# Optimization experiments

Measured on AMD Instinct MI355X. Metric: run time of the kernel, lower is better.

Reference implementation:

```python
import jax, jax.numpy as jnp
import numpy as np

B, S, HID = 2, 2048, 2048
H, HKV, DH = 32, 8, 64
GROUPS = H // HKV
SCALE = DH ** -0.5
ROPE_THETA = 10000.0
NEG_INF = jnp.finfo(jnp.float32).min


def setup_inputs() -> dict:
    key = jax.random.key(0)
    ks = jax.random.split(key, 6)
    hidden_states = jax.random.normal(ks[0], (B, S, HID), dtype=jnp.float32)
    # true rotary embeddings (HF Llama style): inv_freq over half dim, duplicated
    inv_freq = 1.0 / (ROPE_THETA ** (np.arange(0, DH, 2, dtype=np.float32) / DH))
    freqs = np.arange(S, dtype=np.float32)[:, None] * inv_freq[None, :]  # [S, DH/2]
    emb = np.concatenate([freqs, freqs], axis=-1)                        # [S, DH]
    cos = jnp.broadcast_to(jnp.asarray(np.cos(emb), jnp.float32), (B, S, DH))
    sin = jnp.broadcast_to(jnp.asarray(np.sin(emb), jnp.float32), (B, S, DH))
    # additive causal mask [1,1,S,S]
    causal = jnp.tril(jnp.ones((S, S), dtype=bool))
    attention_mask = jnp.where(causal, 0.0, NEG_INF)[None, None].astype(jnp.float32)
    std = 0.02
    Wq = jax.random.normal(ks[1], (H * DH, HID), dtype=jnp.float32) * std
    Wk = jax.random.normal(ks[2], (HKV * DH, HID), dtype=jnp.float32) * std
    Wv = jax.random.normal(ks[3], (HKV * DH, HID), dtype=jnp.float32) * std
    Wo = jax.random.normal(ks[4], (HID, H * DH), dtype=jnp.float32) * std
    return {"hidden_states": hidden_states, "cos": cos, "sin": sin,
            "attention_mask": attention_mask, "Wq": Wq, "Wk": Wk, "Wv": Wv, "Wo": Wo}


def _rotate_half(x):
    x1, x2 = jnp.split(x, 2, axis=-1)
    return jnp.concatenate([-x2, x1], axis=-1)


def reference(hidden_states, cos, sin, attention_mask, Wq, Wk, Wv, Wo):
    b, s, _ = hidden_states.shape
    # projections -> [B, H(kv), S, DH]
    q = (hidden_states @ Wq.T).reshape(b, s, H, DH).transpose(0, 2, 1, 3)
    k = (hidden_states @ Wk.T).reshape(b, s, HKV, DH).transpose(0, 2, 1, 3)
    v = (hidden_states @ Wv.T).reshape(b, s, HKV, DH).transpose(0, 2, 1, 3)
    # RoPE (cos/sin: [B,S,DH] -> broadcast over head axis)
    c = cos[:, None, :, :]
    sn = sin[:, None, :, :]
    q = q * c + _rotate_half(q) * sn
    k = k * c + _rotate_half(k) * sn
    # GQA: repeat kv heads
    k = jnp.repeat(k, GROUPS, axis=1)  # [B,H,S,DH]
    v = jnp.repeat(v, GROUPS, axis=1)
    # eager attention: full [B,H,S,S] scores in memory
    scores = jnp.einsum('bhqd,bhkd->bhqk', q, k) * SCALE + attention_mask[:, :, :, :s]
    attn = jax.nn.softmax(scores, axis=-1)
    out = jnp.einsum('bhqk,bhkd->bhqd', attn, v)
    out = out.transpose(0, 2, 1, 3).reshape(b, s, H * DH)
    return out @ Wo.T
```

## Files before the change

### kernel.cpp

```cpp
#include <hip/hip_runtime.h>
#include <hip/hip_bf16.h>
#include <cstdint>
#include <cstddef>

#define B_    2
#define S_    2048
#define HID_  2048
#define H_    32
#define HKV_  8
#define DH_   64
#define SC2_  0.1803368801111244f

typedef __bf16 bf16;
typedef bf16  bf16x2 __attribute__((ext_vector_type(2)));
typedef bf16  bf16x4 __attribute__((ext_vector_type(4)));
typedef bf16  bf16x8 __attribute__((ext_vector_type(8)));
typedef float f32x4  __attribute__((ext_vector_type(4)));
typedef float f32x16 __attribute__((ext_vector_type(16)));

typedef __attribute__((address_space(3))) uint32_t  lds_u32_t;
typedef __attribute__((address_space(1))) const uint32_t glob_u32_t;

__device__ __forceinline__ void async16(const void* g, void* l) {
    __builtin_amdgcn_global_load_lds((glob_u32_t*)g, (lds_u32_t*)l, 16, 0, 0);
}

__device__ __forceinline__ bf16x8 cvt8(float4 a, float4 b) {
    bf16x8 r;
    r[0] = (bf16)a.x; r[1] = (bf16)a.y; r[2] = (bf16)a.z; r[3] = (bf16)a.w;
    r[4] = (bf16)b.x; r[5] = (bf16)b.y; r[6] = (bf16)b.z; r[7] = (bf16)b.w;
    return r;
}

__device__ __forceinline__ uint32_t pkbf(float a, float b) {
    bf16x2 t; t[0] = (bf16)a; t[1] = (bf16)b;
    return __builtin_bit_cast(uint32_t, t);
}
__device__ __forceinline__ bf16x8 mk8(uint32_t a, uint32_t b, uint32_t c, uint32_t d) {
    union { uint32_t u[4]; bf16x8 v; } t;
    t.u[0] = a; t.u[1] = b; t.u[2] = c; t.u[3] = d;
    return t.v;
}

__global__ __launch_bounds__(256) void cvt_all_kernel(
    const float* __restrict__ X,  const float* __restrict__ Wq,
    const float* __restrict__ Wk, const float* __restrict__ Wv,
    const float* __restrict__ Wo,
    bf16* __restrict__ Xb,  bf16* __restrict__ Wqb, bf16* __restrict__ Wkb,
    bf16* __restrict__ Wvb, bf16* __restrict__ Wob)
{
    const int i = blockIdx.x * 256 + threadIdx.x;
    const float* src; bf16* dst; int off;
    if (i < 1048576)      { src = X;  dst = Xb;  off = i; }
    else if (i < 1572864) { src = Wq; dst = Wqb; off = i - 1048576; }
    else if (i < 1703936) { src = Wk; dst = Wkb; off = i - 1572864; }
    else if (i < 1835008) { src = Wv; dst = Wvb; off = i - 1703936; }
    else                  { src = Wo; dst = Wob; off = i - 1835008; }
    float4 a = ((const float4*)src)[2 * off];
    float4 b = ((const float4*)src)[2 * off + 1];
    ((bf16x8*)dst)[off] = cvt8(a, b);
}

__global__ __launch_bounds__(256) void gemm_qkv_kernel(
    const bf16* __restrict__ A,
    const bf16* __restrict__ Wqb, const bf16* __restrict__ Wkb,
    const bf16* __restrict__ Wvb,
    const float* __restrict__ cs, const float* __restrict__ sn,
    bf16* __restrict__ Qo, bf16* __restrict__ Ko, bf16* __restrict__ Vt)
{
    __shared__ bf16 a_lds[128 * 64];
    __shared__ bf16 b_lds[128 * 64];

    const int tid  = threadIdx.x;
    const int wave = tid >> 6;
    const int lane = tid & 63;
    const int quad = lane >> 4;
    const int l16  = lane & 15;
    const int wm   = wave >> 1;
    const int wn   = wave & 1;
    const int m0   = blockIdx.x * 128;
    const int n0   = blockIdx.y * 128;

    f32x4 acc[4][4];
    #pragma unroll
    for (int mt = 0; mt < 4; ++mt)
        #pragma unroll
        for (int nt = 0; nt < 4; ++nt)
            acc[mt][nt] = (f32x4){0.f, 0.f, 0.f, 0.f};

    int srow[4], sgcol[4];
    const bf16* browp[4];
    #pragma unroll
    for (int i = 0; i < 4; ++i) {
        const int e = tid * 8 + i * 2048;
        srow[i] = e >> 6;
        const int chunk = (e >> 3) & 7;
        sgcol[i] = (chunk ^ (srow[i] & 7)) << 3;
        const int n = n0 + srow[i];
        browp[i] = (n < 2048) ? (Wqb + (size_t)n * HID_)
                 : (n < 2560) ? (Wkb + (size_t)(n - 2048) * HID_)
                              : (Wvb + (size_t)(n - 2560) * HID_);
    }

    for (int k0 = 0; k0 < HID_; k0 += 64) {
        #pragma unroll
        for (int i = 0; i < 4; ++i) {
            async16(A + (size_t)(m0 + srow[i]) * HID_ + k0 + sgcol[i],
                    &a_lds[tid * 8 + i * 2048]);
            async16(browp[i] + k0 + sgcol[i],
                    &b_lds[tid * 8 + i * 2048]);
        }
        __syncthreads();
        #pragma unroll
        for (int ks = 0; ks < 2; ++ks) {
            bf16x8 af[4], bfr[4];
            #pragma unroll
            for (int mt = 0; mt < 4; ++mt) {
                const int row = wm * 64 + mt * 16 + l16;
                const int c = (ks * 4 + quad) ^ (row & 7);
                af[mt] = *(const bf16x8*)(&a_lds[row * 64 + c * 8]);
            }
            #pragma unroll
            for (int nt = 0; nt < 4; ++nt) {
                const int row = wn * 64 + nt * 16 + l16;
                const int c = (ks * 4 + quad) ^ (row & 7);
                bfr[nt] = *(const bf16x8*)(&b_lds[row * 64 + c * 8]);
            }
            #pragma unroll
            for (int mt = 0; mt < 4; ++mt)
                #pragma unroll
                for (int nt = 0; nt < 4; ++nt)
                    acc[mt][nt] = __builtin_amdgcn_mfma_f32_16x16x32_bf16(
                        af[mt], bfr[nt], acc[mt][nt], 0, 0, 0);
        }
        __syncthreads();
    }

    const int nw = n0 + wn * 64;
    const int d  = l16;
    #pragma unroll
    for (int mt = 0; mt < 4; ++mt) {
        #pragma unroll
        for (int r = 0; r < 4; ++r) {
            const int m  = m0 + wm * 64 + mt * 16 + quad * 4 + r;
            const int bb = m >> 11;
            const int ss = m & (S_ - 1);
            const float v0 = acc[mt][0][r], v1 = acc[mt][1][r];
            const float v2 = acc[mt][2][r], v3 = acc[mt][3][r];
            if (nw < 2048) {
                const int h = nw >> 6;
                bf16* dp = Qo + ((size_t)(bb * H_ + h) * S_ + ss) * DH_;
                const float* cp = cs + ((size_t)bb * S_ + ss) * DH_;
                const float* sp = sn + ((size_t)bb * S_ + ss) * DH_;
                dp[ 0 + d] = (bf16)(v0 * cp[ 0 + d] - v2 * sp[ 0 + d]);
                dp[16 + d] = (bf16)(v1 * cp[16 + d] - v3 * sp[16 + d]);
                dp[32 + d] = (bf16)(v2 * cp[32 + d] + v0 * sp[32 + d]);
                dp[48 + d] = (bf16)(v3 * cp[48 + d] + v1 * sp[48 + d]);
            } else if (nw < 2560) {
                const int h = (nw - 2048) >> 6;
                bf16* dp = Ko + ((size_t)(bb * HKV_ + h) * S_ + ss) * DH_;
                const float* cp = cs + ((size_t)bb * S_ + ss) * DH_;
                const float* sp = sn + ((size_t)bb * S_ + ss) * DH_;
                dp[ 0 + d] = (bf16)(v0 * cp[ 0 + d] - v2 * sp[ 0 + d]);
                dp[16 + d] = (bf16)(v1 * cp[16 + d] - v3 * sp[16 + d]);
                dp[32 + d] = (bf16)(v2 * cp[32 + d] + v0 * sp[32 + d]);
                dp[48 + d] = (bf16)(v3 * cp[48 + d] + v1 * sp[48 + d]);
            } else {
                const int h = (nw - 2560) >> 6;
                bf16* dp = Vt + ((size_t)(bb * HKV_ + h) * DH_) * S_ + ss;
                dp[(size_t)( 0 + d) * S_] = (bf16)v0;
                dp[(size_t)(16 + d) * S_] = (bf16)v1;
                dp[(size_t)(32 + d) * S_] = (bf16)v2;
                dp[(size_t)(48 + d) * S_] = (bf16)v3;
            }
        }
    }
}

__global__ __launch_bounds__(256) void gemm_out_kernel(
    const bf16* __restrict__ A, const bf16* __restrict__ Wb,
    float* __restrict__ Y)
{
    __shared__ bf16 a_lds[128 * 64];
    __shared__ bf16 b_lds[128 * 64];

    const int tid  = threadIdx.x;
    const int wave = tid >> 6;
    const int lane = tid & 63;
    const int quad = lane >> 4;
    const int l16  = lane & 15;
    const int wm   = wave >> 1;
    const int wn   = wave & 1;
    const int m0   = blockIdx.x * 128;
    const int n0   = blockIdx.y * 128;

    f32x4 acc[4][4];
    #pragma unroll
    for (int mt = 0; mt < 4; ++mt)
        #pragma unroll
        for (int nt = 0; nt < 4; ++nt)
            acc[mt][nt] = (f32x4){0.f, 0.f, 0.f, 0.f};

    int srow[4], sgcol[4];
    #pragma unroll
    for (int i = 0; i < 4; ++i) {
        const int e = tid * 8 + i * 2048;
        srow[i] = e >> 6;
        const int chunk = (e >> 3) & 7;
        sgcol[i] = (chunk ^ (srow[i] & 7)) << 3;
    }

    for (int k0 = 0; k0 < HID_; k0 += 64) {
        #pragma unroll
        for (int i = 0; i < 4; ++i) {
            async16(A + (size_t)(m0 + srow[i]) * HID_ + k0 + sgcol[i],
                    &a_lds[tid * 8 + i * 2048]);
            async16(Wb + (size_t)(n0 + srow[i]) * HID_ + k0 + sgcol[i],
                    &b_lds[tid * 8 + i * 2048]);
        }
        __syncthreads();
        #pragma unroll
        for (int ks = 0; ks < 2; ++ks) {
            bf16x8 af[4], bfr[4];
            #pragma unroll
            for (int mt = 0; mt < 4; ++mt) {
                const int row = wm * 64 + mt * 16 + l16;
                const int c = (ks * 4 + quad) ^ (row & 7);
                af[mt] = *(const bf16x8*)(&a_lds[row * 64 + c * 8]);
            }
            #pragma unroll
            for (int nt = 0; nt < 4; ++nt) {
                const int row = wn * 64 + nt * 16 + l16;
                const int c = (ks * 4 + quad) ^ (row & 7);
                bfr[nt] = *(const bf16x8*)(&b_lds[row * 64 + c * 8]);
            }
            #pragma unroll
            for (int mt = 0; mt < 4; ++mt)
                #pragma unroll
                for (int nt = 0; nt < 4; ++nt)
                    acc[mt][nt] = __builtin_amdgcn_mfma_f32_16x16x32_bf16(
                        af[mt], bfr[nt], acc[mt][nt], 0, 0, 0);
        }
        __syncthreads();
    }

    #pragma unroll
    for (int mt = 0; mt < 4; ++mt)
        #pragma unroll
        for (int nt = 0; nt < 4; ++nt)
            #pragma unroll
            for (int r = 0; r < 4; ++r) {
                const int m = m0 + wm * 64 + mt * 16 + quad * 4 + r;
                const int n = n0 + wn * 64 + nt * 16 + l16;
                Y[(size_t)m * HID_ + n] = acc[mt][nt][r];
            }
}

__global__ __launch_bounds__(256) void attn_kernel(
    const bf16* __restrict__ Q, const bf16* __restrict__ K,
    const bf16* __restrict__ Vt, bf16* __restrict__ O)
{
    __shared__ bf16 k_lds[2][64 * 64];
    __shared__ bf16 v_lds[2][64 * 64];

    const int tid  = threadIdx.x;
    const int wave = tid >> 6;
    const int lane = tid & 63;
    const int l32  = lane & 31;
    const int half = lane >> 5;
    const int h  = blockIdx.y;
    const int b  = blockIdx.z;
    const int hkv = h >> 2;

    const bf16* Qg = Q  + (size_t)(b * H_ + h) * S_ * DH_;
    const bf16* Kg = K  + (size_t)(b * HKV_ + hkv) * S_ * DH_;
    const bf16* Vg = Vt + ((size_t)(b * HKV_ + hkv) * DH_) * S_;

    const int srow0  = tid >> 3;
    const int scolsw = ((tid & 7) ^ ((tid >> 3) & 7)) << 3;

    #pragma unroll 1
    for (int ph = 0; ph < 2; ++ph) {
        const int qt  = ph == 0 ? (int)blockIdx.x : (15 - (int)blockIdx.x);
        const int q0  = qt * 128;
        const int qb0 = q0 + wave * 32;
        const int qa  = qb0 + l32;

        bf16x8 qf[4];
        #pragma unroll
        for (int c = 0; c < 4; ++c)
            qf[c] = *(const bf16x8*)(Qg + (size_t)(qb0 + l32) * DH_ + c * 16 + half * 8);

        f32x16 o_acc[2];
        #pragma unroll
        for (int dt = 0; dt < 2; ++dt)
            #pragma unroll
            for (int e = 0; e < 16; ++e) o_acc[dt][e] = 0.f;
        float m_i = -1e30f, l_i = 0.f;

        const int nkt = 2 * qt + 2;

        #pragma unroll
        for (int i = 0; i < 2; ++i) {
            const int row = srow0 + i * 32;
            async16(Kg + (size_t)row * DH_ + scolsw, &k_lds[0][tid * 8 + i * 2048]);
            async16(Vg + (size_t)row * S_  + scolsw, &v_lds[0][tid * 8 + i * 2048]);
        }
        __syncthreads();

        for (int kt = 0; kt < nkt; ++kt) {
            if (kt + 1 < nkt) {
                bf16* kb = k_lds[(kt + 1) & 1];
                bf16* vb = v_lds[(kt + 1) & 1];
                #pragma unroll
                for (int i = 0; i < 2; ++i) {
                    const int row = srow0 + i * 32;
                    async16(Kg + (size_t)((kt + 1) * 64 + row) * DH_ + scolsw,
                            kb + tid * 8 + i * 2048);
                    async16(Vg + (size_t)row * S_ + (kt + 1) * 64 + scolsw,
                            vb + tid * 8 + i * 2048);
                }
            }

            if (kt * 64 <= qb0 + 31) {
                const bf16* kb = k_lds[kt & 1];
                const bf16* vb = v_lds[kt & 1];
                const bool act1 = (kt * 64 + 32) <= (qb0 + 31);

                bf16x8 vf[2][4];
                #pragma unroll
                for (int dt = 0; dt < 2; ++dt)
                    #pragma unroll
                    for (int c = 0; c < 4; ++c) {
                        const int row = dt * 32 + l32;
                        const int col = ((2 * c + half) ^ (row & 7)) << 3;
                        vf[dt][c] = *(const bf16x8*)(vb + row * 64 + col);
                    }

                f32x16 s0, s1;
                {
                    bf16x8 kf[4];
                    #pragma unroll
                    for (int c = 0; c < 4; ++c) {
                        const int row = l32;
                        const int col = ((2 * c + half) ^ (row & 7)) << 3;
                        kf[c] = *(const bf16x8*)(kb + row * 64 + col);
                    }
                    f32x16 a;
                    #pragma unroll
                    for (int e = 0; e < 16; ++e) a[e] = 0.f;
                    #pragma unroll
                    for (int c = 0; c < 4; ++c)
                        a = __builtin_amdgcn_mfma_f32_32x32x16_bf16(kf[c], qf[c], a, 0, 0, 0);
                    s0 = a;
                }
                if (act1) {
                    bf16x8 kf[4];
                    #pragma unroll
                    for (int c = 0; c < 4; ++c) {
                        const int row = 32 + l32;
                        const int col = ((2 * c + half) ^ (row & 7)) << 3;
                        kf[c] = *(const bf16x8*)(kb + row * 64 + col);
                    }
                    f32x16 a;
                    #pragma unroll
                    for (int e = 0; e < 16; ++e) a[e] = 0.f;
                    #pragma unroll
                    for (int c = 0; c < 4; ++c)
                        a = __builtin_amdgcn_mfma_f32_32x32x16_bf16(kf[c], qf[c], a, 0, 0, 0);
                    s1 = a;
                }

                {
                    const bool full0 = (kt * 64 + 31) <= qb0;
                    #pragma unroll
                    for (int e = 0; e < 16; ++e) {
                        float v = s0[e] * SC2_;
                        if (!full0) {
                            const int kp = kt * 64 + (e & 3) + 8 * (e >> 2) + 4 * half;
                            v = (kp <= qa) ? v : -1e30f;
                        }
                        s0[e] = v;
                    }
                }
                if (act1) {
                    const bool full1 = (kt * 64 + 63) <= qb0;
                    #pragma unroll
                    for (int e = 0; e < 16; ++e) {
                        float v = s1[e] * SC2_;
                        if (!full1) {
                            const int kp = kt * 64 + 32 + (e & 3) + 8 * (e >> 2) + 4 * half;
                            v = (kp <= qa) ? v : -1e30f;
                        }
                        s1[e] = v;
                    }
                }

                float mx = -1e30f;
                #pragma unroll
                for (int e = 0; e < 16; ++e) mx = fmaxf(mx, s0[e]);
                if (act1)
                    #pragma unroll
                    for (int e = 0; e < 16; ++e) mx = fmaxf(mx, s1[e]);
                mx = fmaxf(mx, __shfl_xor(mx, 32));
                const float mn = fmaxf(m_i, mx);
                const float al = exp2f(m_i - mn);
                m_i = mn;
                float sm = 0.f;
                #pragma unroll
                for (int e = 0; e < 16; ++e) {
                    const float p = exp2f(s0[e] - mn);
                    s0[e] = p; sm += p;
                }
                if (act1)
                    #pragma unroll
                    for (int e = 0; e < 16; ++e) {
                        const float p = exp2f(s1[e] - mn);
                        s1[e] = p; sm += p;
                    }
                sm += __shfl_xor(sm, 32);
                l_i = l_i * al + sm;
                #pragma unroll
                for (int dt = 0; dt < 2; ++dt)
                    #pragma unroll
                    for (int e = 0; e < 16; ++e) o_acc[dt][e] *= al;

                bf16x8 pf[4];
                {
                    uint32_t d0 = pkbf(s0[0],  s0[1]),  d1 = pkbf(s0[2],  s0[3]);
                    uint32_t d2 = pkbf(s0[4],  s0[5]),  d3 = pkbf(s0[6],  s0[7]);
                    uint32_t d4 = pkbf(s0[8],  s0[9]),  d5 = pkbf(s0[10], s0[11]);
                    uint32_t d6 = pkbf(s0[12], s0[13]), d7 = pkbf(s0[14], s0[15]);
                    uint32_t x0 = __shfl_xor((int)d0, 32), x1 = __shfl_xor((int)d1, 32);
                    uint32_t x2 = __shfl_xor((int)d2, 32), x3 = __shfl_xor((int)d3, 32);
                    uint32_t x4 = __shfl_xor((int)d4, 32), x5 = __shfl_xor((int)d5, 32);
                    uint32_t x6 = __shfl_xor((int)d6, 32), x7 = __shfl_xor((int)d7, 32);
                    pf[0] = half ? mk8(x2, x3, d2, d3) : mk8(d0, d1, x0, x1);
                    pf[1] = half ? mk8(x6, x7, d6, d7) : mk8(d4, d5, x4, x5);
                }
                if (act1) {
                    uint32_t d0 = pkbf(s1[0],  s1[1]),  d1 = pkbf(s1[2],  s1[3]);
                    uint32_t d2 = pkbf(s1[4],  s1[5]),  d3 = pkbf(s1[6],  s1[7]);
                    uint32_t d4 = pkbf(s1[8],  s1[9]),  d5 = pkbf(s1[10], s1[11]);
                    uint32_t d6 = pkbf(s1[12], s1[13]), d7 = pkbf(s1[14], s1[15]);
                    uint32_t x0 = __shfl_xor((int)d0, 32), x1 = __shfl_xor((int)d1, 32);
                    uint32_t x2 = __shfl_xor((int)d2, 32), x3 = __shfl_xor((int)d3, 32);
                    uint32_t x4 = __shfl_xor((int)d4, 32), x5 = __shfl_xor((int)d5, 32);
                    uint32_t x6 = __shfl_xor((int)d6, 32), x7 = __shfl_xor((int)d7, 32);
                    pf[2] = half ? mk8(x2, x3, d2, d3) : mk8(d0, d1, x0, x1);
                    pf[3] = half ? mk8(x6, x7, d6, d7) : mk8(d4, d5, x4, x5);
                }

                const int nc = act1 ? 4 : 2;
                #pragma unroll
                for (int c = 0; c < 4; ++c) {
                    if (c >= nc) break;
                    #pragma unroll
                    for (int dt = 0; dt < 2; ++dt)
                        o_acc[dt] = __builtin_amdgcn_mfma_f32_32x32x16_bf16(
                            vf[dt][c], pf[c], o_acc[dt], 0, 0, 0);
                }
            }
            __syncthreads();
        }

        const float inv = 1.f / l_i;
        bf16* op = O + ((size_t)(b * S_ + qa) * H_ + h) * DH_;
        #pragma unroll
        for (int dt = 0; dt < 2; ++dt)
            #pragma unroll
            for (int g = 0; g < 4; ++g) {
                bf16x4 ov;
                #pragma unroll
                for (int r = 0; r < 4; ++r) ov[r] = (bf16)(o_acc[dt][g * 4 + r] * inv);
                *(bf16x4*)(op + dt * 32 + g * 8 + half * 4) = ov;
            }
        __syncthreads();
    }
}

extern "C" void kernel_launch(void* const* d_in, const int* in_sizes, int n_in,
                              void* d_out, int out_size, void* d_ws, size_t ws_size,
                              hipStream_t stream)
{
    const float* X    = (const float*)d_in[0];
    const float* cs   = (const float*)d_in[1];
    const float* sn   = (const float*)d_in[2];
    const float* Wq   = (const float*)d_in[4];
    const float* Wk   = (const float*)d_in[5];
    const float* Wv   = (const float*)d_in[6];
    const float* Wo   = (const float*)d_in[7];
    float* Y          = (float*)d_out;

    bf16* Xb  = (bf16*)d_ws;
    bf16* Wqb = Xb  + (size_t)8388608;
    bf16* Wkb = Wqb + (size_t)4194304;
    bf16* Wvb = Wkb + (size_t)1048576;
    bf16* Wob = Wvb + (size_t)1048576;
    bf16* Qb  = Wob + (size_t)4194304;
    bf16* Kb  = Qb  + (size_t)8388608;
    bf16* Vtb = Kb  + (size_t)2097152;
    bf16* Ob  = Vtb + (size_t)2097152;

    dim3 blk(256);
    cvt_all_kernel<<<dim3(9216), blk, 0, stream>>>(X, Wq, Wk, Wv, Wo,
                                                   Xb, Wqb, Wkb, Wvb, Wob);
    gemm_qkv_kernel<<<dim3(32, 24), blk, 0, stream>>>(Xb, Wqb, Wkb, Wvb,
                                                      cs, sn, Qb, Kb, Vtb);
    attn_kernel<<<dim3(8, H_, B_), blk, 0, stream>>>(Qb, Kb, Vtb, Ob);
    gemm_out_kernel<<<dim3(32, 16), blk, 0, stream>>>(Ob, Wob, Y);
}
```

Before: 372.4 us.

## Rebalance causal attention work per block, fold softmax scale into Q, lazy rescale

The attention kernel now pairs a low and a high 64-row query tile inside each block, so every block does a uniform amount of K/V work. The two-phase loop is removed and the grid doubles to 16 blocks in x, with launch bounds asking for 4 blocks per CU. The softmax scale is folded into Q during the QKV GEMM epilogue, which removes a per-score multiply. Masking is simplified, the running-max rescale is skipped when the max grows by no more than 8, and the half-wave shuffle exchange is replaced with permlane32_swap. The risks are more register pressure from the occupancy hint and tiny numeric differences from the lazy rescale threshold.

```diff
diff --git a/kernel.cpp b/kernel.cpp
--- a/kernel.cpp
+++ b/kernel.cpp
@@ -17,6 +17,7 @@
 typedef bf16  bf16x8 __attribute__((ext_vector_type(8)));
 typedef float f32x4  __attribute__((ext_vector_type(4)));
 typedef float f32x16 __attribute__((ext_vector_type(16)));
+typedef uint32_t u32x2 __attribute__((ext_vector_type(2)));
 
 typedef __attribute__((address_space(3))) uint32_t  lds_u32_t;
 typedef __attribute__((address_space(1))) const uint32_t glob_u32_t;
@@ -152,10 +153,10 @@
                 bf16* dp = Qo + ((size_t)(bb * H_ + h) * S_ + ss) * DH_;
                 const float* cp = cs + ((size_t)bb * S_ + ss) * DH_;
                 const float* sp = sn + ((size_t)bb * S_ + ss) * DH_;
-                dp[ 0 + d] = (bf16)(v0 * cp[ 0 + d] - v2 * sp[ 0 + d]);
-                dp[16 + d] = (bf16)(v1 * cp[16 + d] - v3 * sp[16 + d]);
-                dp[32 + d] = (bf16)(v2 * cp[32 + d] + v0 * sp[32 + d]);
-                dp[48 + d] = (bf16)(v3 * cp[48 + d] + v1 * sp[48 + d]);
+                dp[ 0 + d] = (bf16)((v0 * cp[ 0 + d] - v2 * sp[ 0 + d]) * SC2_);
+                dp[16 + d] = (bf16)((v1 * cp[16 + d] - v3 * sp[16 + d]) * SC2_);
+                dp[32 + d] = (bf16)((v2 * cp[32 + d] + v0 * sp[32 + d]) * SC2_);
+                dp[48 + d] = (bf16)((v3 * cp[48 + d] + v1 * sp[48 + d]) * SC2_);
             } else if (nw < 2560) {
                 const int h = (nw - 2048) >> 6;
                 bf16* dp = Ko + ((size_t)(bb * HKV_ + h) * S_ + ss) * DH_;
@@ -256,7 +257,7 @@
             }
 }
 
-__global__ __launch_bounds__(256) void attn_kernel(
+__global__ __launch_bounds__(256, 4) void attn_kernel(
     const bf16* __restrict__ Q, const bf16* __restrict__ K,
     const bf16* __restrict__ Vt, bf16* __restrict__ O)
 {
@@ -279,204 +280,192 @@
     const int srow0  = tid >> 3;
     const int scolsw = ((tid & 7) ^ ((tid >> 3) & 7)) << 3;
 
-    #pragma unroll 1
-    for (int ph = 0; ph < 2; ++ph) {
-        const int qt  = ph == 0 ? (int)blockIdx.x : (15 - (int)blockIdx.x);
-        const int q0  = qt * 128;
-        const int qb0 = q0 + wave * 32;
-        const int qa  = qb0 + l32;
-
-        bf16x8 qf[4];
-        #pragma unroll
-        for (int c = 0; c < 4; ++c)
-            qf[c] = *(const bf16x8*)(Qg + (size_t)(qb0 + l32) * DH_ + c * 16 + half * 8);
-
-        f32x16 o_acc[2];
-        #pragma unroll
-        for (int dt = 0; dt < 2; ++dt)
-            #pragma unroll
-            for (int e = 0; e < 16; ++e) o_acc[dt][e] = 0.f;
-        float m_i = -1e30f, l_i = 0.f;
-
-        const int nkt = 2 * qt + 2;
-
-        #pragma unroll
-        for (int i = 0; i < 2; ++i) {
-            const int row = srow0 + i * 32;
-            async16(Kg + (size_t)row * DH_ + scolsw, &k_lds[0][tid * 8 + i * 2048]);
-            async16(Vg + (size_t)row * S_  + scolsw, &v_lds[0][tid * 8 + i * 2048]);
-        }
-        __syncthreads();
-
-        for (int kt = 0; kt < nkt; ++kt) {
-            if (kt + 1 < nkt) {
-                bf16* kb = k_lds[(kt + 1) & 1];
-                bf16* vb = v_lds[(kt + 1) & 1];
-                #pragma unroll
-                for (int i = 0; i < 2; ++i) {
-                    const int row = srow0 + i * 32;
-                    async16(Kg + (size_t)((kt + 1) * 64 + row) * DH_ + scolsw,
-                            kb + tid * 8 + i * 2048);
-                    async16(Vg + (size_t)row * S_ + (kt + 1) * 64 + scolsw,
-                            vb + tid * 8 + i * 2048);
+    const int p   = blockIdx.x;
+    const int st  = (wave < 2) ? p : (31 - p);
+    const int qb0 = st * 64 + (wave & 1) * 32;
+    const int qa  = qb0 + l32;
+    const int nkt = 32 - p;
+
+    bf16x8 qf[4];
+    #pragma unroll
+    for (int c = 0; c < 4; ++c)
+        qf[c] = *(const bf16x8*)(Qg + (size_t)qa * DH_ + c * 16 + half * 8);
+
+    f32x16 o_acc[2];
+    #pragma unroll
+    for (int dt = 0; dt < 2; ++dt)
+        #pragma unroll
+        for (int e = 0; e < 16; ++e) o_acc[dt][e] = 0.f;
+    float m_i = -1e30f, l_i = 0.f;
+
+    #pragma unroll
+    for (int i = 0; i < 2; ++i) {
+        const int row = srow0 + i * 32;
+        async16(Kg + (size_t)row * DH_ + scolsw, &k_lds[0][tid * 8 + i * 2048]);
+        async16(Vg + (size_t)row * S_  + scolsw, &v_lds[0][tid * 8 + i * 2048]);
+    }
+    __syncthreads();
+
+    for (int kt = 0; kt < nkt; ++kt) {
+        if (kt + 1 < nkt) {
+            bf16* kb = k_lds[(kt + 1) & 1];
+            bf16* vb = v_lds[(kt + 1) & 1];
+            #pragma unroll
+            for (int i = 0; i < 2; ++i) {
+                const int row = srow0 + i * 32;
+                async16(Kg + (size_t)((kt + 1) * 64 + row) * DH_ + scolsw,
+                        kb + tid * 8 + i * 2048);
+                async16(Vg + (size_t)row * S_ + (kt + 1) * 64 + scolsw,
+                        vb + tid * 8 + i * 2048);
+            }
+        }
+
+        if (kt * 64 <= qb0 + 31) {
+            const bf16* kb = k_lds[kt & 1];
+            const bf16* vb = v_lds[kt & 1];
+            const bool act1 = (kt * 64 + 32) <= (qb0 + 31);
+
+            bf16x8 vf[2][4];
+            #pragma unroll
+            for (int dt = 0; dt < 2; ++dt)
+                #pragma unroll
+                for (int c = 0; c < 4; ++c) {
+                    const int row = dt * 32 + l32;
+                    const int col = ((2 * c + half) ^ (row & 7)) << 3;
+                    vf[dt][c] = *(const bf16x8*)(vb + row * 64 + col);
                 }
-            }
-
-            if (kt * 64 <= qb0 + 31) {
-                const bf16* kb = k_lds[kt & 1];
-                const bf16* vb = v_lds[kt & 1];
-                const bool act1 = (kt * 64 + 32) <= (qb0 + 31);
-
-                bf16x8 vf[2][4];
-                #pragma unroll
-                for (int dt = 0; dt < 2; ++dt)
-                    #pragma unroll
-                    for (int c = 0; c < 4; ++c) {
-                        const int row = dt * 32 + l32;
-                        const int col = ((2 * c + half) ^ (row & 7)) << 3;
-                        vf[dt][c] = *(const bf16x8*)(vb + row * 64 + col);
-                    }
-
-                f32x16 s0, s1;
-                {
-                    bf16x8 kf[4];
-                    #pragma unroll
-                    for (int c = 0; c < 4; ++c) {
-                        const int row = l32;
-                        const int col = ((2 * c + half) ^ (row & 7)) << 3;
-                        kf[c] = *(const bf16x8*)(kb + row * 64 + col);
-                    }
-                    f32x16 a;
-                    #pragma unroll
-                    for (int e = 0; e < 16; ++e) a[e] = 0.f;
-                    #pragma unroll
-                    for (int c = 0; c < 4; ++c)
-                        a = __builtin_amdgcn_mfma_f32_32x32x16_bf16(kf[c], qf[c], a, 0, 0, 0);
-                    s0 = a;
+
+            f32x16 s0, s1;
+            {
+                bf16x8 kf[4];
+                #pragma unroll
+                for (int c = 0; c < 4; ++c) {
+                    const int row = l32;
+                    const int col = ((2 * c + half) ^ (row & 7)) << 3;
+                    kf[c] = *(const bf16x8*)(kb + row * 64 + col);
                 }
-                if (act1) {
-                    bf16x8 kf[4];
-                    #pragma unroll
-                    for (int c = 0; c < 4; ++c) {
-                        const int row = 32 + l32;
-                        const int col = ((2 * c + half) ^ (row & 7)) << 3;
-                        kf[c] = *(const bf16x8*)(kb + row * 64 + col);
-                    }
-                    f32x16 a;
-                    #pragma unroll
-                    for (int e = 0; e < 16; ++e) a[e] = 0.f;
-                    #pragma unroll
-                    for (int c = 0; c < 4; ++c)
-                        a = __builtin_amdgcn_mfma_f32_32x32x16_bf16(kf[c], qf[c], a, 0, 0, 0);
-                    s1 = a;
+                f32x16 a;
+                #pragma unroll
+                for (int e = 0; e < 16; ++e) a[e] = 0.f;
+                #pragma unroll
+                for (int c = 0; c < 4; ++c)
+                    a = __builtin_amdgcn_mfma_f32_32x32x16_bf16(kf[c], qf[c], a, 0, 0, 0);
+                s0 = a;
+            }
+            if (act1) {
+                bf16x8 kf[4];
+                #pragma unroll
+                for (int c = 0; c < 4; ++c) {
+                    const int row = 32 + l32;
+                    const int col = ((2 * c + half) ^ (row & 7)) << 3;
+                    kf[c] = *(const bf16x8*)(kb + row * 64 + col);
                 }
-
-                {
-                    const bool full0 = (kt * 64 + 31) <= qb0;
-                    #pragma unroll
-                    for (int e = 0; e < 16; ++e) {
-                        float v = s0[e] * SC2_;
-                        if (!full0) {
-                            const int kp = kt * 64 + (e & 3) + 8 * (e >> 2) + 4 * half;
-                            v = (kp <= qa) ? v : -1e30f;
-                        }
-                        s0[e] = v;
-                    }
-                }
-                if (act1) {
-                    const bool full1 = (kt * 64 + 63) <= qb0;
-                    #pragma unroll
-                    for (int e = 0; e < 16; ++e) {
-                        float v = s1[e] * SC2_;
-                        if (!full1) {
-                            const int kp = kt * 64 + 32 + (e & 3) + 8 * (e >> 2) + 4 * half;
-                            v = (kp <= qa) ? v : -1e30f;
-                        }
-                        s1[e] = v;
-                    }
-                }
-
-                float mx = -1e30f;
-                #pragma unroll
-                for (int e = 0; e < 16; ++e) mx = fmaxf(mx, s0[e]);
-                if (act1)
-                    #pragma unroll
-                    for (int e = 0; e < 16; ++e) mx = fmaxf(mx, s1[e]);
-                mx = fmaxf(mx, __shfl_xor(mx, 32));
+                f32x16 a;
+                #pragma unroll
+                for (int e = 0; e < 16; ++e) a[e] = 0.f;
+                #pragma unroll
+                for (int c = 0; c < 4; ++c)
+                    a = __builtin_amdgcn_mfma_f32_32x32x16_bf16(kf[c], qf[c], a, 0, 0, 0);
+                s1 = a;
+            }
+
+            if (!((kt * 64 + 31) <= qb0)) {
+                const int qrel = qa - kt * 64 - 4 * half;
+                #pragma unroll
+                for (int e = 0; e < 16; ++e)
+                    if (((e & 3) + 8 * (e >> 2)) > qrel) s0[e] = -1e30f;
+            }
+            if (act1 && !((kt * 64 + 63) <= qb0)) {
+                const int qrel = qa - kt * 64 - 32 - 4 * half;
+                #pragma unroll
+                for (int e = 0; e < 16; ++e)
+                    if (((e & 3) + 8 * (e >> 2)) > qrel) s1[e] = -1e30f;
+            }
+
+            float mx = s0[0];
+            #pragma unroll
+            for (int e = 1; e < 16; ++e) mx = fmaxf(mx, s0[e]);
+            if (act1)
+                #pragma unroll
+                for (int e = 0; e < 16; ++e) mx = fmaxf(mx, s1[e]);
+            mx = fmaxf(mx, __shfl_xor(mx, 32));
+
+            float al = 1.f;
+            if (!__all(mx <= m_i + 8.f)) {
                 const float mn = fmaxf(m_i, mx);
-                const float al = exp2f(m_i - mn);
+                al = exp2f(m_i - mn);
                 m_i = mn;
-                float sm = 0.f;
-                #pragma unroll
-                for (int e = 0; e < 16; ++e) {
-                    const float p = exp2f(s0[e] - mn);
-                    s0[e] = p; sm += p;
-                }
-                if (act1)
-                    #pragma unroll
-                    for (int e = 0; e < 16; ++e) {
-                        const float p = exp2f(s1[e] - mn);
-                        s1[e] = p; sm += p;
-                    }
-                sm += __shfl_xor(sm, 32);
-                l_i = l_i * al + sm;
                 #pragma unroll
                 for (int dt = 0; dt < 2; ++dt)
                     #pragma unroll
                     for (int e = 0; e < 16; ++e) o_acc[dt][e] *= al;
-
-                bf16x8 pf[4];
-                {
-                    uint32_t d0 = pkbf(s0[0],  s0[1]),  d1 = pkbf(s0[2],  s0[3]);
-                    uint32_t d2 = pkbf(s0[4],  s0[5]),  d3 = pkbf(s0[6],  s0[7]);
-                    uint32_t d4 = pkbf(s0[8],  s0[9]),  d5 = pkbf(s0[10], s0[11]);
-                    uint32_t d6 = pkbf(s0[12], s0[13]), d7 = pkbf(s0[14], s0[15]);
-                    uint32_t x0 = __shfl_xor((int)d0, 32), x1 = __shfl_xor((int)d1, 32);
-                    uint32_t x2 = __shfl_xor((int)d2, 32), x3 = __shfl_xor((int)d3, 32);
-                    uint32_t x4 = __shfl_xor((int)d4, 32), x5 = __shfl_xor((int)d5, 32);
-                    uint32_t x6 = __shfl_xor((int)d6, 32), x7 = __shfl_xor((int)d7, 32);
-                    pf[0] = half ? mk8(x2, x3, d2, d3) : mk8(d0, d1, x0, x1);
-                    pf[1] = half ? mk8(x6, x7, d6, d7) : mk8(d4, d5, x4, x5);
+            }
+
+            float sm = 0.f;
+            #pragma unroll
+            for (int e = 0; e < 16; ++e) {
+                const float pp = exp2f(s0[e] - m_i);
+                s0[e] = pp; sm += pp;
+            }
+            if (act1)
+                #pragma unroll
+                for (int e = 0; e < 16; ++e) {
+                    const float pp = exp2f(s1[e] - m_i);
+                    s1[e] = pp; sm += pp;
                 }
-                if (act1) {
-                    uint32_t d0 = pkbf(s1[0],  s1[1]),  d1 = pkbf(s1[2],  s1[3]);
-                    uint32_t d2 = pkbf(s1[4],  s1[5]),  d3 = pkbf(s1[6],  s1[7]);
-                    uint32_t d4 = pkbf(s1[8],  s1[9]),  d5 = pkbf(s1[10], s1[11]);
-                    uint32_t d6 = pkbf(s1[12], s1[13]), d7 = pkbf(s1[14], s1[15]);
-                    uint32_t x0 = __shfl_xor((int)d0, 32), x1 = __shfl_xor((int)d1, 32);
-                    uint32_t x2 = __shfl_xor((int)d2, 32), x3 = __shfl_xor((int)d3, 32);
-                    uint32_t x4 = __shfl_xor((int)d4, 32), x5 = __shfl_xor((int)d5, 32);
-                    uint32_t x6 = __shfl_xor((int)d6, 32), x7 = __shfl_xor((int)d7, 32);
-                    pf[2] = half ? mk8(x2, x3, d2, d3) : mk8(d0, d1, x0, x1);
-                    pf[3] = half ? mk8(x6, x7, d6, d7) : mk8(d4, d5, x4, x5);
-                }
-
-                const int nc = act1 ? 4 : 2;
-                #pragma unroll
-                for (int c = 0; c < 4; ++c) {
-                    if (c >= nc) break;
-                    #pragma unroll
-                    for (int dt = 0; dt < 2; ++dt)
-                        o_acc[dt] = __builtin_amdgcn_mfma_f32_32x32x16_bf16(
-                            vf[dt][c], pf[c], o_acc[dt], 0, 0, 0);
-                }
-            }
-            __syncthreads();
-        }
-
-        const float inv = 1.f / l_i;
-        bf16* op = O + ((size_t)(b * S_ + qa) * H_ + h) * DH_;
-        #pragma unroll
-        for (int dt = 0; dt < 2; ++dt)
-            #pragma unroll
-            for (int g = 0; g < 4; ++g) {
-                bf16x4 ov;
-                #pragma unroll
-                for (int r = 0; r < 4; ++r) ov[r] = (bf16)(o_acc[dt][g * 4 + r] * inv);
-                *(bf16x4*)(op + dt * 32 + g * 8 + half * 4) = ov;
-            }
+            sm += __shfl_xor(sm, 32);
+            l_i = l_i * al + sm;
+
+            bf16x8 pf[4];
+            {
+                uint32_t d0 = pkbf(s0[0],  s0[1]),  d1 = pkbf(s0[2],  s0[3]);
+                uint32_t d2 = pkbf(s0[4],  s0[5]),  d3 = pkbf(s0[6],  s0[7]);
+                uint32_t d4 = pkbf(s0[8],  s0[9]),  d5 = pkbf(s0[10], s0[11]);
+                uint32_t d6 = pkbf(s0[12], s0[13]), d7 = pkbf(s0[14], s0[15]);
+                u32x2 r02 = __builtin_amdgcn_permlane32_swap(d0, d2, false, false);
+                u32x2 r13 = __builtin_amdgcn_permlane32_swap(d1, d3, false, false);
+                u32x2 r46 = __builtin_amdgcn_permlane32_swap(d4, d6, false, false);
+                u32x2 r57 = __builtin_amdgcn_permlane32_swap(d5, d7, false, false);
+                pf[0] = mk8(r02[0], r13[0], r02[1], r13[1]);
+                pf[1] = mk8(r46[0], r57[0], r46[1], r57[1]);
+            }
+            if (act1) {
+                uint32_t d0 = pkbf(s1[0],  s1[1]),  d1 = pkbf(s1[2],  s1[3]);
+                uint32_t d2 = pkbf(s1[4],  s1[5]),  d3 = pkbf(s1[6],  s1[7]);
+                uint32_t d4 = pkbf(s1[8],  s1[9]),  d5 = pkbf(s1[10], s1[11]);
+                uint32_t d6 = pkbf(s1[12], s1[13]), d7 = pkbf(s1[14], s1[15]);
+                u32x2 r02 = __builtin_amdgcn_permlane32_swap(d0, d2, false, false);
+                u32x2 r13 = __builtin_amdgcn_permlane32_swap(d1, d3, false, false);
+                u32x2 r46 = __builtin_amdgcn_permlane32_swap(d4, d6, false, false);
+                u32x2 r57 = __builtin_amdgcn_permlane32_swap(d5, d7, false, false);
+                pf[2] = mk8(r02[0], r13[0], r02[1], r13[1]);
+                pf[3] = mk8(r46[0], r57[0], r46[1], r57[1]);
+            }
+
+            const int nc = act1 ? 4 : 2;
+            #pragma unroll
+            for (int c = 0; c < 4; ++c) {
+                if (c >= nc) break;
+                #pragma unroll
+                for (int dt = 0; dt < 2; ++dt)
+                    o_acc[dt] = __builtin_amdgcn_mfma_f32_32x32x16_bf16(
+                        vf[dt][c], pf[c], o_acc[dt], 0, 0, 0);
+            }
+        }
         __syncthreads();
     }
+
+    const float inv = 1.f / l_i;
+    bf16* op = O + ((size_t)(b * S_ + qa) * H_ + h) * DH_;
+    #pragma unroll
+    for (int dt = 0; dt < 2; ++dt)
+        #pragma unroll
+        for (int g = 0; g < 4; ++g) {
+            bf16x4 ov;
+            #pragma unroll
+            for (int r = 0; r < 4; ++r) ov[r] = (bf16)(o_acc[dt][g * 4 + r] * inv);
+            *(bf16x4*)(op + dt * 32 + g * 8 + half * 4) = ov;
+        }
 }
 
 extern "C" void kernel_launch(void* const* d_in, const int* in_sizes, int n_in,
@@ -507,6 +496,6 @@
                                                    Xb, Wqb, Wkb, Wvb, Wob);
     gemm_qkv_kernel<<<dim3(32, 24), blk, 0, stream>>>(Xb, Wqb, Wkb, Wvb,
                                                       cs, sn, Qb, Kb, Vtb);
-    attn_kernel<<<dim3(8, H_, B_), blk, 0, stream>>>(Qb, Kb, Vtb, Ob);
+    attn_kernel<<<dim3(16, H_, B_), blk, 0, stream>>>(Qb, Kb, Vtb, Ob);
     gemm_out_kernel<<<dim3(32, 16), blk, 0, stream>>>(Ob, Wob, Y);
 }
```

New measurement: 410.2 us. 1.1x slower.
